# Optimization experiments

Measured on AMD Instinct MI355X. Metric: run time of the kernel, lower is better.

The kernel has to match this reference:

```python
import jax, jax.numpy as jnp
import numpy as np

DIM = 1024
N_HEADS = 16
HEAD_DIM = DIM // N_HEADS
MLP_DIM = 4096
B, L, M = 4, 1024, 1024
EPS = 1e-5


def _mha(q_in, k_in, v_in, mask, wq, wk, wv, wo):
    b, l, d = q_in.shape
    m = k_in.shape[1]
    # torch view(b, l, head_dim, n_heads): split last dim as (head_dim, n_heads)
    q = (q_in @ wq).reshape(b, l, HEAD_DIM, N_HEADS)
    k = (k_in @ wk).reshape(b, m, HEAD_DIM, N_HEADS)
    v = (v_in @ wv).reshape(b, m, HEAD_DIM, N_HEADS)  # computed but unused downstream (source quirk)
    score = jnp.einsum('bldn,bmdn->blmn', q, k)
    # source applies mask BEFORE scaling
    score = jnp.where(mask, jnp.float32(-1e9), score)
    score = score / (HEAD_DIM ** 0.5)
    attn = jax.nn.softmax(score, axis=2)
    # SOURCE QUIRK: second einsum uses k, not v — reproduced faithfully
    x = jnp.einsum('blmn,bmdn->bldn', attn, k)
    x = x.reshape(b, l, d)  # 'b l d n -> b l (d n)'
    return x @ wo


def _layer_norm(x, g, b):
    mu = jnp.mean(x, axis=-1, keepdims=True)
    var = jnp.var(x, axis=-1, keepdims=True)
    return (x - mu) * jax.lax.rsqrt(var + EPS) * g + b


def setup_inputs() -> dict:
    key = jax.random.key(0)
    ks = jax.random.split(key, 16)
    s = 0.02
    inp = {
        'x': jax.random.normal(ks[0], (B, L, DIM), dtype=jnp.float32),
        'enc_output': jax.random.normal(ks[1], (B, M, DIM), dtype=jnp.float32),
        # causal mask: True above diagonal => masked
        'self_attn_mask': jnp.triu(jnp.ones((L, L), dtype=bool), k=1)[None, :, :, None],
        'enc_dec_mask': jnp.zeros((1, L, M, 1), dtype=bool),
        'sa_wq': s * jax.random.normal(ks[2], (DIM, DIM), jnp.float32),
        'sa_wk': s * jax.random.normal(ks[3], (DIM, DIM), jnp.float32),
        'sa_wv': s * jax.random.normal(ks[4], (DIM, DIM), jnp.float32),
        'sa_wo': s * jax.random.normal(ks[5], (DIM, DIM), jnp.float32),
        'ca_wq': s * jax.random.normal(ks[6], (DIM, DIM), jnp.float32),
        'ca_wk': s * jax.random.normal(ks[7], (DIM, DIM), jnp.float32),
        'ca_wv': s * jax.random.normal(ks[8], (DIM, DIM), jnp.float32),
        'ca_wo': s * jax.random.normal(ks[9], (DIM, DIM), jnp.float32),
        'ln1_g': jnp.ones((DIM,), jnp.float32), 'ln1_b': jnp.zeros((DIM,), jnp.float32),
        'ln2_g': jnp.ones((DIM,), jnp.float32), 'ln2_b': jnp.zeros((DIM,), jnp.float32),
        'ln3_g': jnp.ones((DIM,), jnp.float32), 'ln3_b': jnp.zeros((DIM,), jnp.float32),
        'ff_w1': s * jax.random.normal(ks[10], (DIM, MLP_DIM), jnp.float32),
        'ff_b1': jnp.zeros((MLP_DIM,), jnp.float32),
        'ff_w2': s * jax.random.normal(ks[11], (MLP_DIM, DIM), jnp.float32),
        'ff_b2': jnp.zeros((DIM,), jnp.float32),
    }
    return inp


def reference(x, enc_output, self_attn_mask, enc_dec_mask,
              sa_wq, sa_wk, sa_wv, sa_wo,
              ca_wq, ca_wk, ca_wv, ca_wo,
              ln1_g, ln1_b, ln2_g, ln2_b, ln3_g, ln3_b,
              ff_w1, ff_b1, ff_w2, ff_b2):
    # self-attention + residual + LN (dropout = identity in eval)
    h = x + _mha(x, x, x, self_attn_mask, sa_wq, sa_wk, sa_wv, sa_wo)
    h = _layer_norm(h, ln1_g, ln1_b)
    # encoder-decoder attention + residual + LN
    h = h + _mha(h, enc_output, enc_output, enc_dec_mask, ca_wq, ca_wk, ca_wv, ca_wo)
    h = _layer_norm(h, ln2_g, ln2_b)
    # position-wise FFN (gelu, exact erf like torch default) + residual + LN
    ff = jax.nn.gelu(h @ ff_w1 + ff_b1, approximate=False) @ ff_w2 + ff_b2
    h = h + ff
    h = _layer_norm(h, ln3_g, ln3_b)
    return h
```

## Files before the change

### kernel.cpp

```cpp
#include <hip/hip_runtime.h>
#include <hip/hip_bf16.h>
#include <stdint.h>

typedef unsigned short u16;
typedef _Float16 f16x8 __attribute__((ext_vector_type(8)));
typedef float f32x4 __attribute__((ext_vector_type(4)));

#define TOK 4096

__device__ __forceinline__ u16 f2h(float f) {
  _Float16 h = (_Float16)f;
  return __builtin_bit_cast(unsigned short, h);
}
__device__ __forceinline__ float h2f(u16 b) {
  return (float)__builtin_bit_cast(_Float16, b);
}
__device__ __forceinline__ unsigned pack2(float a, float b) {
  return (unsigned)f2h(a) | ((unsigned)f2h(b) << 16);
}
__device__ __forceinline__ void gld16(const u16* g, u16* l) {
  __builtin_amdgcn_global_load_lds(
      (const __attribute__((address_space(1))) void*)g,
      (__attribute__((address_space(3))) void*)l, 16, 0, 0);
}
__device__ __forceinline__ float gelu_fast(float v) {
  float z = 1.5957691216f * v * (1.0f + 0.044715f * v * v);
  return v / (1.0f + __expf(-z));
}

__device__ __forceinline__ void tc_body(const float* W, u16* Wt, int K, int N,
                                        int bx, int by, int tid) {
  __shared__ float tile[32][33];
  int n0 = bx * 32, k0 = by * 32;
  int tx = tid & 31, ty = tid >> 5;
#pragma unroll
  for (int e = 0; e < 4; e++)
    tile[ty + e * 8][tx] = W[(size_t)(k0 + ty + e * 8) * N + n0 + tx];
  __syncthreads();
#pragma unroll
  for (int e = 0; e < 4; e++)
    Wt[(size_t)(n0 + ty + e * 8) * K + k0 + tx] = f2h(tile[tx][ty + e * 8]);
}
__device__ __forceinline__ void cast_body(const float* in, u16* out, int blk, int tid) {
  int i = blk * 256 + tid;
  const float4* p = (const float4*)(in + (size_t)i * 8);
  float4 a = p[0], b = p[1];
  uint4 o;
  o.x = pack2(a.x, a.y); o.y = pack2(a.z, a.w);
  o.z = pack2(b.x, b.y); o.w = pack2(b.z, b.w);
  *(uint4*)(out + (size_t)i * 8) = o;
}

__global__ __launch_bounds__(256) void prep_kernel(
    const float* x, const float* enc, u16* xh, u16* ench,
    const float* W0, const float* W1, const float* W2,
    const float* W3, const float* W4, const float* W5,
    u16* T0, u16* T1, u16* T2, u16* T3, u16* T4, u16* T5,
    const float* Wff1, u16* Tff1, const float* Wff2, u16* Tff2) {
  int blk = blockIdx.x, tid = threadIdx.x;
  if (blk < 2048) { cast_body(x, xh, blk, tid); return; }
  if (blk < 4096) { cast_body(enc, ench, blk - 2048, tid); return; }
  if (blk < 10240) {
    int t = blk - 4096;
    int z = t >> 10, s = t & 1023;
    const float* W; u16* T;
    switch (z) {
      case 0: W = W0; T = T0; break;
      case 1: W = W1; T = T1; break;
      case 2: W = W2; T = T2; break;
      case 3: W = W3; T = T3; break;
      case 4: W = W4; T = T4; break;
      default: W = W5; T = T5; break;
    }
    tc_body(W, T, 1024, 1024, s & 31, s >> 5, tid);
    return;
  }
  if (blk < 14336) {
    int t = blk - 10240;
    tc_body(Wff1, Tff1, 1024, 4096, t & 127, t >> 7, tid);
    return;
  }
  {
    int t = blk - 14336;
    tc_body(Wff2, Tff2, 4096, 1024, t & 31, t >> 5, tid);
  }
}

template <int EPI, int BN, int BK>
__global__ __launch_bounds__((BN == 256) ? 512 : 256)
void gemm_bt_kernel(const u16* __restrict__ A0,
                    const u16* __restrict__ A1,
                    const u16* __restrict__ Bt,
                    u16* __restrict__ Cb0,
                    u16* __restrict__ Cb1,
                    u16* __restrict__ CbT,
                    const float* __restrict__ bias,
                    int M, int N, int K, int KLEN) {
  constexpr int SWM = BK / 8 - 1;
  __shared__ u16 As[2][128 * BK];
  __shared__ u16 Bs[2][BN * BK];
  int tid = threadIdx.x, lane = tid & 63, wid = tid >> 6;
  int gx = gridDim.x, gy = gridDim.y;
  int nwg = gx * gy;
  int flat = blockIdx.x + gx * blockIdx.y;
  int k8 = flat & 7, idx = flat >> 3;
  int bx, by;
  if (gx >= 16) {
    int rx = gx >> 2, ry = gy >> 1;
    int kx = k8 & 3, ky = k8 >> 2;
    bx = kx * rx + idx % rx;
    by = ky * ry + idx / rx;
  } else {
    int widx = k8 * (nwg >> 3) + idx;
    bx = widx % gx;
    by = widx / gx;
  }
  int row0 = by * 128, col0 = bx * BN;
  bool is_k = (EPI == 0) && (col0 >= 1024);
  const u16* A = is_k ? A1 : A0;
  int wm = (BN == 256) ? (wid >> 2) * 64 : (wid >> 1) * 64;
  int wn = (BN == 256) ? (wid & 3) * 64 : (wid & 1) * 64;
  size_t koff = (EPI == 4) ? (size_t)blockIdx.z * KLEN : 0;
  int ra = lane & 15, kg = lane >> 4;

  const u16 *Ab0, *Ab1, *Bb0, *Bb1;
  int srow = 0, ssw = 0;
  if constexpr (BK == 64) {
    srow = wid * 8 + (lane >> 3);
    ssw = (lane & 7) ^ ((srow >> 1) & 7);
    Ab0 = A + (size_t)(row0 + srow) * K + koff + ssw * 8;
    Bb0 = Bt + (size_t)(col0 + srow) * K + koff + ssw * 8;
    Ab1 = nullptr; Bb1 = nullptr;
  } else {
    int sr = tid >> 2;
    int scol = (((tid & 3) ^ ((sr >> 1) & 3)) * 8);
    Ab0 = A + (size_t)(row0 + sr) * K + koff + scol;
    Ab1 = A + (size_t)(row0 + 64 + sr) * K + koff + scol;
    Bb0 = Bt + (size_t)(col0 + sr) * K + koff + scol;
    Bb1 = Bt + (size_t)(col0 + ((BN == 256) ? 128 : 64) + sr) * K + koff + scol;
  }

  f32x4 acc[4][4];
#pragma unroll
  for (int i = 0; i < 4; i++)
#pragma unroll
    for (int j = 0; j < 4; j++) { acc[i][j][0] = 0.f; acc[i][j][1] = 0.f; acc[i][j][2] = 0.f; acc[i][j][3] = 0.f; }
  int KT = KLEN / BK;
  int arow[4], asw[4], brow[4], bsw[4];
#pragma unroll
  for (int i = 0; i < 4; i++) {
    arow[i] = wm + i * 16 + ra;
    asw[i] = (arow[i] >> 1) & SWM;
    brow[i] = wn + i * 16 + ra;
    bsw[i] = (brow[i] >> 1) & SWM;
  }

  auto STAGE = [&](int kt, int buf) {
    if constexpr (BK == 64) {
#pragma unroll
      for (int i = 0; i < 4; i++) {
        gld16(Ab0 + (size_t)i * 32 * K + kt * 64, &As[buf][i * 2048 + wid * 512]);
        gld16(Bb0 + (size_t)i * 32 * K + kt * 64, &Bs[buf][i * 2048 + wid * 512]);
      }
    } else if constexpr (BN == 256) {
      gld16(Ab0 + kt * 32, &As[buf][wid * 512]);
      gld16(Bb0 + kt * 32, &Bs[buf][wid * 512]);
      gld16(Bb1 + kt * 32, &Bs[buf][4096 + wid * 512]);
    } else {
      gld16(Ab0 + kt * 32, &As[buf][wid * 512]);
      gld16(Ab1 + kt * 32, &As[buf][2048 + wid * 512]);
      gld16(Bb0 + kt * 32, &Bs[buf][wid * 512]);
      gld16(Bb1 + kt * 32, &Bs[buf][2048 + wid * 512]);
    }
  };

  STAGE(0, 0);
  __syncthreads();
  int cur = 0;
  for (int kt = 0; kt < KT; ++kt) {
    if (kt + 1 < KT) STAGE(kt + 1, cur ^ 1);
#pragma unroll
    for (int kk = 0; kk < BK / 32; kk++) {
      f16x8 af[4], bfv[4];
#pragma unroll
      for (int i = 0; i < 4; i++)
        af[i] = *(const f16x8*)&As[cur][arow[i] * BK + (((kk * 4 + kg) ^ asw[i]) * 8)];
#pragma unroll
      for (int j = 0; j < 4; j++)
        bfv[j] = *(const f16x8*)&Bs[cur][brow[j] * BK + (((kk * 4 + kg) ^ bsw[j]) * 8)];
#pragma unroll
      for (int i = 0; i < 4; i++)
#pragma unroll
        for (int j = 0; j < 4; j++)
          acc[i][j] = __builtin_amdgcn_mfma_f32_16x16x32_f16(af[i], bfv[j], acc[i][j], 0, 0, 0);
    }
    __syncthreads();
    cur ^= 1;
  }

  int rq = kg * 4;
#pragma unroll
  for (int i = 0; i < 4; i++) {
    int rowb = row0 + wm + i * 16 + rq;
    if (EPI == 0) {
      int b = rowb >> 10, l0 = rowb & 1023;
      int d0 = ((col0 + wn) >> 4) & 63;
      size_t hb = ((size_t)(b * 16 + ra)) * 1024;
      u16* dst = is_k ? Cb1 : Cb0;
      u16 h[4][4];
#pragma unroll
      for (int j = 0; j < 4; j++)
#pragma unroll
        for (int q = 0; q < 4; q++) h[j][q] = f2h(acc[i][j][q]);
#pragma unroll
      for (int q = 0; q < 4; q++) {
        ushort4 hv;
        hv.x = h[0][q]; hv.y = h[1][q]; hv.z = h[2][q]; hv.w = h[3][q];
        *(ushort4*)&dst[(hb + l0 + q) * 64 + d0] = hv;
      }
      if (is_k) {
#pragma unroll
        for (int j = 0; j < 4; j++) {
          uint2 ov;
          ov.x = (unsigned)h[j][0] | ((unsigned)h[j][1] << 16);
          ov.y = (unsigned)h[j][2] | ((unsigned)h[j][3] << 16);
          *(uint2*)&CbT[((size_t)(b * 16 + ra)) * 65536 + ((size_t)(d0 + j)) * 1024 + l0] = ov;
        }
      }
    } else {
#pragma unroll
      for (int j = 0; j < 4; j++) {
        int col = col0 + wn + j * 16 + ra;
        float bval = 0.f;
        if (EPI == 2) bval = bias[col];
        if (EPI == 4 && blockIdx.z == 0 && bias) bval = bias[col];
#pragma unroll
        for (int q = 0; q < 4; q++) {
          int row = rowb + q;
          float v = acc[i][j][q] + bval;
          if (EPI == 2) {
            Cb0[(size_t)row * N + col] = f2h(gelu_fast(v));
          } else {
            Cb0[(size_t)blockIdx.z * M * N + (size_t)row * N + col] = f2h(v);
          }
        }
      }
    }
  }
}

template <bool CAUSAL>
__global__ __launch_bounds__(256) void flash3_kernel(const u16* __restrict__ Qh,
                                                     const u16* __restrict__ Kh,
                                                     const u16* __restrict__ KhT,
                                                     u16* __restrict__ Xtok) {
  const int L = 1024;
  int tid = threadIdx.x, lane = tid & 63, wid = tid >> 6;
  int gx = gridDim.x, nwg = gx * gridDim.y;
  int flat = blockIdx.x + gx * blockIdx.y;
  int widx = (flat & 7) * (nwg >> 3) + (flat >> 3);
  int qt = widx % gx, bh = widx / gx;
  if (CAUSAL) qt = gx - 1 - qt;
  __shared__ u16 Ks[2][4096];
  __shared__ u16 Kt[2][4096];
  __shared__ u16 Ps[4][2048];
  int ra = lane & 15, kg = lane >> 4;
  int rq = kg * 4;
  int wr0 = qt * 128 + wid * 32;
  f16x8 qa[2][2];
#pragma unroll
  for (int i = 0; i < 2; i++) {
    const u16* Qb = Qh + ((size_t)bh * L + wr0 + i * 16 + ra) * 64;
    qa[i][0] = *(const f16x8*)(Qb + kg * 8);
    qa[i][1] = *(const f16x8*)(Qb + 32 + kg * 8);
  }
  f32x4 oacc[2][4];
#pragma unroll
  for (int i = 0; i < 2; i++)
#pragma unroll
    for (int d = 0; d < 4; d++) { oacc[i][d][0] = 0.f; oacc[i][d][1] = 0.f; oacc[i][d][2] = 0.f; oacc[i][d][3] = 0.f; }
  float l_i[2][4];
#pragma unroll
  for (int i = 0; i < 2; i++)
#pragma unroll
    for (int q = 0; q < 4; q++) l_i[i][q] = 0.f;
  int ntiles = CAUSAL ? (2 * qt + 2) : 16;
  int fr = lane >> 3, fc = lane & 7;

#define KSTAGE(mt, buf) do {                                                        \
    {                                                                               \
      int rr = wid * 8 + fr;                                                        \
      int cc = fc ^ fr;                                                             \
      gld16(Kh + ((size_t)bh * L + (mt) * 64 + rr) * 64 + cc * 8, &Ks[buf][wid * 512]);          \
      gld16(KhT + ((size_t)bh * 64 + rr) * L + (size_t)(mt) * 64 + cc * 8, &Kt[buf][wid * 512]); \
    }                                                                               \
    {                                                                               \
      int rr = 32 + wid * 8 + fr;                                                   \
      int cc = fc ^ fr;                                                             \
      gld16(Kh + ((size_t)bh * L + (mt) * 64 + rr) * 64 + cc * 8, &Ks[buf][2048 + wid * 512]);          \
      gld16(KhT + ((size_t)bh * 64 + rr) * L + (size_t)(mt) * 64 + cc * 8, &Kt[buf][2048 + wid * 512]); \
    }                                                                               \
  } while (0)

  KSTAGE(0, 0);
  __syncthreads();
  int cur = 0;
  for (int mt = 0; mt < ntiles; ++mt) {
    if (mt + 1 < ntiles) KSTAGE(mt + 1, cur ^ 1);
    bool active = !(CAUSAL && (wr0 + 31 < mt * 64));
    if (active) {
      bool wmask = CAUSAL && (mt * 64 + 63 > wr0);
      float p[2][4][4];
      __builtin_amdgcn_s_setprio(1);
#pragma unroll
      for (int j = 0; j < 4; j++) {
        int krow = j * 16 + ra;
        int s2 = krow & 7;
        f16x8 kb0 = *(const f16x8*)&Ks[cur][krow * 64 + ((kg ^ s2) * 8)];
        f16x8 kb1 = *(const f16x8*)&Ks[cur][krow * 64 + (((4 + kg) ^ s2) * 8)];
#pragma unroll
        for (int i = 0; i < 2; i++) {
          f32x4 a; a[0] = 0.f; a[1] = 0.f; a[2] = 0.f; a[3] = 0.f;
          a = __builtin_amdgcn_mfma_f32_16x16x32_f16(qa[i][0], kb0, a, 0, 0, 0);
          a = __builtin_amdgcn_mfma_f32_16x16x32_f16(qa[i][1], kb1, a, 0, 0, 0);
#pragma unroll
          for (int q = 0; q < 4; q++) {
            float v = a[q] * 0.125f;
            if (wmask) {
              int rg = wr0 + i * 16 + rq + q;
              int cg = mt * 64 + j * 16 + ra;
              if (cg > rg) v = -1.25e8f;
            }
            p[i][j][q] = __expf(v);
          }
        }
      }
      __builtin_amdgcn_s_setprio(0);
#pragma unroll
      for (int i = 0; i < 2; i++) {
        float rs[4] = {0.f, 0.f, 0.f, 0.f};
#pragma unroll
        for (int j = 0; j < 4; j++)
#pragma unroll
          for (int q = 0; q < 4; q++) rs[q] += p[i][j][q];
#pragma unroll
        for (int off = 1; off < 16; off <<= 1)
#pragma unroll
          for (int q = 0; q < 4; q++) rs[q] += __shfl_xor(rs[q], off);
#pragma unroll
        for (int q = 0; q < 4; q++) l_i[i][q] += rs[q];
      }
#pragma unroll
      for (int i = 0; i < 2; i++)
#pragma unroll
        for (int j = 0; j < 4; j++)
#pragma unroll
          for (int q = 0; q < 4; q++) {
            int prow = i * 16 + rq + q;
            int pcol = j * 16 + ra;
            Ps[wid][prow * 64 + (((pcol >> 3) ^ (prow & 7)) * 8) + (pcol & 7)] = f2h(p[i][j][q]);
          }
      f16x8 pa[2][2];
#pragma unroll
      for (int i = 0; i < 2; i++) {
        int arow = i * 16 + ra;
        int s3 = arow & 7;
        pa[i][0] = *(const f16x8*)&Ps[wid][arow * 64 + ((kg ^ s3) * 8)];
        pa[i][1] = *(const f16x8*)&Ps[wid][arow * 64 + (((4 + kg) ^ s3) * 8)];
      }
      __builtin_amdgcn_s_setprio(1);
#pragma unroll
      for (int d = 0; d < 4; d++) {
        int krow = d * 16 + ra;
        int s4 = krow & 7;
        f16x8 kc0 = *(const f16x8*)&Kt[cur][krow * 64 + ((kg ^ s4) * 8)];
        f16x8 kc1 = *(const f16x8*)&Kt[cur][krow * 64 + (((4 + kg) ^ s4) * 8)];
#pragma unroll
        for (int i = 0; i < 2; i++) {
          oacc[i][d] = __builtin_amdgcn_mfma_f32_16x16x32_f16(pa[i][0], kc0, oacc[i][d], 0, 0, 0);
          oacc[i][d] = __builtin_amdgcn_mfma_f32_16x16x32_f16(pa[i][1], kc1, oacc[i][d], 0, 0, 0);
        }
      }
      __builtin_amdgcn_s_setprio(0);
    }
    __syncthreads();
    cur ^= 1;
  }
#undef KSTAGE
  int b = bh >> 4, nh = bh & 15;
#pragma unroll
  for (int i = 0; i < 2; i++)
#pragma unroll
    for (int q = 0; q < 4; q++) {
      float inv = 1.0f / l_i[i][q];
      int l = wr0 + i * 16 + rq + q;
      size_t rowg = ((size_t)b * 1024 + l) * 1024;
#pragma unroll
      for (int d = 0; d < 4; d++)
        Xtok[rowg + (d * 16 + ra) * 16 + nh] = f2h(oacc[i][d][q] * inv);
    }
}

template <int WRITE_H, int P>
__global__ __launch_bounds__(256) void ln_kernel(const u16* __restrict__ parts,
                                                 const float* __restrict__ res,
                                                 const float* __restrict__ g,
                                                 const float* __restrict__ bb,
                                                 float* __restrict__ outf,
                                                 u16* __restrict__ outh) {
  int row = blockIdx.x, tid = threadIdx.x;
  int lane = tid & 63, wid = tid >> 6;
  size_t base = (size_t)row * 1024 + tid * 4;
  float4 vr = *(const float4*)(res + base);
  float x0 = vr.x, x1 = vr.y, x2 = vr.z, x3 = vr.w;
#pragma unroll
  for (int p = 0; p < P; p++) {
    uint2 v = *(const uint2*)&parts[(size_t)p * 4194304 + base];
    x0 += h2f((u16)v.x);
    x1 += h2f((u16)(v.x >> 16));
    x2 += h2f((u16)v.y);
    x3 += h2f((u16)(v.y >> 16));
  }
  float s = x0 + x1 + x2 + x3;
  float sq = x0 * x0 + x1 * x1 + x2 * x2 + x3 * x3;
#pragma unroll
  for (int off = 1; off < 64; off <<= 1) {
    s += __shfl_xor(s, off);
    sq += __shfl_xor(sq, off);
  }
  __shared__ float red[8];
  if (lane == 0) { red[wid] = s; red[4 + wid] = sq; }
  __syncthreads();
  s = red[0] + red[1] + red[2] + red[3];
  sq = red[4] + red[5] + red[6] + red[7];
  float mean = s * (1.0f / 1024.0f);
  float var = sq * (1.0f / 1024.0f) - mean * mean;
  float rstd = rsqrtf(var + 1e-5f);
  float4 vg = *(const float4*)(g + tid * 4);
  float4 vb = *(const float4*)(bb + tid * 4);
  float y0 = (x0 - mean) * rstd * vg.x + vb.x;
  float y1 = (x1 - mean) * rstd * vg.y + vb.y;
  float y2 = (x2 - mean) * rstd * vg.z + vb.z;
  float y3 = (x3 - mean) * rstd * vg.w + vb.w;
  float4 yo; yo.x = y0; yo.y = y1; yo.z = y2; yo.w = y3;
  *(float4*)(outf + base) = yo;
  if (WRITE_H) {
    uint2 ov; ov.x = pack2(y0, y1); ov.y = pack2(y2, y3);
    *(uint2*)(outh + base) = ov;
  }
}

extern "C" void kernel_launch(void* const* d_in, const int* in_sizes, int n_in,
                              void* d_out, int out_size, void* d_ws, size_t ws_size,
                              hipStream_t stream) {
  (void)in_sizes; (void)n_in; (void)out_size; (void)ws_size;
  const float* x    = (const float*)d_in[0];
  const float* enc  = (const float*)d_in[1];
  const float* sa_wq = (const float*)d_in[4];
  const float* sa_wk = (const float*)d_in[5];
  const float* sa_wo = (const float*)d_in[7];
  const float* ca_wq = (const float*)d_in[8];
  const float* ca_wk = (const float*)d_in[9];
  const float* ca_wo = (const float*)d_in[11];
  const float* ln1g = (const float*)d_in[12];
  const float* ln1b = (const float*)d_in[13];
  const float* ln2g = (const float*)d_in[14];
  const float* ln2b = (const float*)d_in[15];
  const float* ln3g = (const float*)d_in[16];
  const float* ln3b = (const float*)d_in[17];
  const float* ffw1 = (const float*)d_in[18];
  const float* ffb1 = (const float*)d_in[19];
  const float* ffw2 = (const float*)d_in[20];
  const float* ffb2 = (const float*)d_in[21];

  uint8_t* w = (uint8_t*)d_ws;
  const size_t MB = 1024ull * 1024ull;
  u16* wt_saqk = (u16*)(w + 0 * MB);
  u16* wt_sao  = (u16*)(w + 4 * MB);
  u16* wt_caqk = (u16*)(w + 6 * MB);
  u16* wt_cao  = (u16*)(w + 10 * MB);
  u16* wt_ff1  = (u16*)(w + 12 * MB);
  u16* wt_ff2  = (u16*)(w + 20 * MB);
  u16* act_h   = (u16*)(w + 28 * MB);
  u16* enc_h   = (u16*)(w + 36 * MB);
  u16* qhd     = (u16*)(w + 44 * MB);
  u16* khd     = (u16*)(w + 52 * MB);
  u16* khdT    = (u16*)(w + 60 * MB);
  u16* ctxtok  = (u16*)(w + 68 * MB);
  u16* parts   = (u16*)(w + 76 * MB);
  float* hA    = (float*)(w + 108 * MB);
  float* hB    = (float*)(w + 124 * MB);
  u16* ff1h = qhd;

  prep_kernel<<<18432, 256, 0, stream>>>(
      x, enc, act_h, enc_h,
      sa_wq, sa_wk, sa_wo, ca_wq, ca_wk, ca_wo,
      wt_saqk, wt_saqk + 1024 * 1024, wt_sao,
      wt_caqk, wt_caqk + 1024 * 1024, wt_cao,
      ffw1, wt_ff1, ffw2, wt_ff2);

  gemm_bt_kernel<0, 128, 64><<<dim3(16, 32, 1), 256, 0, stream>>>(
      act_h, act_h, wt_saqk, qhd, khd, khdT, nullptr, TOK, 2048, 1024, 1024);
  flash3_kernel<true><<<dim3(8, 64), 256, 0, stream>>>(qhd, khd, khdT, ctxtok);
  gemm_bt_kernel<4, 128, 64><<<dim3(8, 32, 2), 256, 0, stream>>>(
      ctxtok, ctxtok, wt_sao, parts, nullptr, nullptr, nullptr, TOK, 1024, 1024, 512);
  ln_kernel<1, 2><<<4096, 256, 0, stream>>>(parts, x, ln1g, ln1b, hA, act_h);

  gemm_bt_kernel<0, 128, 64><<<dim3(16, 32, 1), 256, 0, stream>>>(
      act_h, enc_h, wt_caqk, qhd, khd, khdT, nullptr, TOK, 2048, 1024, 1024);
  flash3_kernel<false><<<dim3(8, 64), 256, 0, stream>>>(qhd, khd, khdT, ctxtok);
  gemm_bt_kernel<4, 128, 64><<<dim3(8, 32, 2), 256, 0, stream>>>(
      ctxtok, ctxtok, wt_cao, parts, nullptr, nullptr, nullptr, TOK, 1024, 1024, 512);
  ln_kernel<1, 2><<<4096, 256, 0, stream>>>(parts, hA, ln2g, ln2b, hB, act_h);

  gemm_bt_kernel<2, 256, 32><<<dim3(16, 32, 1), 512, 0, stream>>>(
      act_h, act_h, wt_ff1, ff1h, nullptr, nullptr, ffb1, TOK, 4096, 1024, 1024);
  gemm_bt_kernel<4, 128, 64><<<dim3(8, 32, 2), 256, 0, stream>>>(
      ff1h, ff1h, wt_ff2, parts, nullptr, nullptr, ffb2, TOK, 1024, 4096, 2048);
  ln_kernel<0, 2><<<4096, 256, 0, stream>>>(parts, hB, ln3g, ln3b, (float*)d_out, nullptr);
}
```

Measured before the change: 332.4 us.

## Split attention work across 8 waves with 16 query rows each

The flash attention kernel now launches 512 threads (8 waves) per 128-row query tile instead of 4 waves of 32 rows. Each wave handles 16 rows, so the cooperative K/K^T tile staging needs one load pair per thread instead of two. The per-tile row-sum shuffle reduction is deferred to the end, with each lane accumulating partial sums locally. This aims for more latency hiding and less per-tile reduction work, at the cost of each K fragment read from LDS being reused by only one MFMA row block instead of two.

Result: faster. 307.9 us (-7.4%).

```diff
diff --git a/kernel.cpp b/kernel.cpp
--- a/kernel.cpp
+++ b/kernel.cpp
@@ -124,10 +124,9 @@
   int ra = lane & 15, kg = lane >> 4;
 
   const u16 *Ab0, *Ab1, *Bb0, *Bb1;
-  int srow = 0, ssw = 0;
   if constexpr (BK == 64) {
-    srow = wid * 8 + (lane >> 3);
-    ssw = (lane & 7) ^ ((srow >> 1) & 7);
+    int srow = wid * 8 + (lane >> 3);
+    int ssw = (lane & 7) ^ ((srow >> 1) & 7);
     Ab0 = A + (size_t)(row0 + srow) * K + koff + ssw * 8;
     Bb0 = Bt + (size_t)(col0 + srow) * K + koff + ssw * 8;
     Ab1 = nullptr; Bb1 = nullptr;
@@ -250,7 +249,7 @@
 }
 
 template <bool CAUSAL>
-__global__ __launch_bounds__(256) void flash3_kernel(const u16* __restrict__ Qh,
+__global__ __launch_bounds__(512) void flash4_kernel(const u16* __restrict__ Qh,
                                                      const u16* __restrict__ Kh,
                                                      const u16* __restrict__ KhT,
                                                      u16* __restrict__ Xtok) {
@@ -263,43 +262,28 @@
   if (CAUSAL) qt = gx - 1 - qt;
   __shared__ u16 Ks[2][4096];
   __shared__ u16 Kt[2][4096];
-  __shared__ u16 Ps[4][2048];
-  int ra = lane & 15, kg = lane >> 4;
-  int rq = kg * 4;
-  int wr0 = qt * 128 + wid * 32;
-  f16x8 qa[2][2];
-#pragma unroll
-  for (int i = 0; i < 2; i++) {
-    const u16* Qb = Qh + ((size_t)bh * L + wr0 + i * 16 + ra) * 64;
-    qa[i][0] = *(const f16x8*)(Qb + kg * 8);
-    qa[i][1] = *(const f16x8*)(Qb + 32 + kg * 8);
-  }
-  f32x4 oacc[2][4];
-#pragma unroll
-  for (int i = 0; i < 2; i++)
-#pragma unroll
-    for (int d = 0; d < 4; d++) { oacc[i][d][0] = 0.f; oacc[i][d][1] = 0.f; oacc[i][d][2] = 0.f; oacc[i][d][3] = 0.f; }
-  float l_i[2][4];
-#pragma unroll
-  for (int i = 0; i < 2; i++)
-#pragma unroll
-    for (int q = 0; q < 4; q++) l_i[i][q] = 0.f;
+  __shared__ u16 Ps[8][1024];
+  int ra = lane & 15, kg = lane >> 4, rq = kg * 4;
+  int wr0 = qt * 128 + wid * 16;
+  f16x8 qa0, qa1;
+  {
+    const u16* Qb = Qh + ((size_t)bh * L + wr0 + ra) * 64;
+    qa0 = *(const f16x8*)(Qb + kg * 8);
+    qa1 = *(const f16x8*)(Qb + 32 + kg * 8);
+  }
+  f32x4 oacc[4];
+#pragma unroll
+  for (int d = 0; d < 4; d++) { oacc[d][0] = 0.f; oacc[d][1] = 0.f; oacc[d][2] = 0.f; oacc[d][3] = 0.f; }
+  float l_acc[4] = {0.f, 0.f, 0.f, 0.f};
   int ntiles = CAUSAL ? (2 * qt + 2) : 16;
   int fr = lane >> 3, fc = lane & 7;
-
-#define KSTAGE(mt, buf) do {                                                        \
-    {                                                                               \
-      int rr = wid * 8 + fr;                                                        \
-      int cc = fc ^ fr;                                                             \
-      gld16(Kh + ((size_t)bh * L + (mt) * 64 + rr) * 64 + cc * 8, &Ks[buf][wid * 512]);          \
-      gld16(KhT + ((size_t)bh * 64 + rr) * L + (size_t)(mt) * 64 + cc * 8, &Kt[buf][wid * 512]); \
-    }                                                                               \
-    {                                                                               \
-      int rr = 32 + wid * 8 + fr;                                                   \
-      int cc = fc ^ fr;                                                             \
-      gld16(Kh + ((size_t)bh * L + (mt) * 64 + rr) * 64 + cc * 8, &Ks[buf][2048 + wid * 512]);          \
-      gld16(KhT + ((size_t)bh * 64 + rr) * L + (size_t)(mt) * 64 + cc * 8, &Kt[buf][2048 + wid * 512]); \
-    }                                                                               \
+  int rr = wid * 8 + fr;
+  int cc_ = fc ^ (rr & 7);
+  int sw = ra & 7;
+
+#define KSTAGE(mt, buf) do {                                                            \
+    gld16(Kh + ((size_t)bh * L + (mt) * 64 + rr) * 64 + cc_ * 8, &Ks[buf][wid * 512]);  \
+    gld16(KhT + ((size_t)bh * 64 + rr) * L + (size_t)(mt) * 64 + cc_ * 8, &Kt[buf][wid * 512]); \
   } while (0)
 
   KSTAGE(0, 0);
@@ -307,79 +291,52 @@
   int cur = 0;
   for (int mt = 0; mt < ntiles; ++mt) {
     if (mt + 1 < ntiles) KSTAGE(mt + 1, cur ^ 1);
-    bool active = !(CAUSAL && (wr0 + 31 < mt * 64));
+    bool active = !(CAUSAL && (wr0 + 15 < mt * 64));
     if (active) {
       bool wmask = CAUSAL && (mt * 64 + 63 > wr0);
-      float p[2][4][4];
+      float p[4][4];
       __builtin_amdgcn_s_setprio(1);
 #pragma unroll
       for (int j = 0; j < 4; j++) {
         int krow = j * 16 + ra;
-        int s2 = krow & 7;
-        f16x8 kb0 = *(const f16x8*)&Ks[cur][krow * 64 + ((kg ^ s2) * 8)];
-        f16x8 kb1 = *(const f16x8*)&Ks[cur][krow * 64 + (((4 + kg) ^ s2) * 8)];
-#pragma unroll
-        for (int i = 0; i < 2; i++) {
-          f32x4 a; a[0] = 0.f; a[1] = 0.f; a[2] = 0.f; a[3] = 0.f;
-          a = __builtin_amdgcn_mfma_f32_16x16x32_f16(qa[i][0], kb0, a, 0, 0, 0);
-          a = __builtin_amdgcn_mfma_f32_16x16x32_f16(qa[i][1], kb1, a, 0, 0, 0);
-#pragma unroll
-          for (int q = 0; q < 4; q++) {
-            float v = a[q] * 0.125f;
-            if (wmask) {
-              int rg = wr0 + i * 16 + rq + q;
-              int cg = mt * 64 + j * 16 + ra;
-              if (cg > rg) v = -1.25e8f;
-            }
-            p[i][j][q] = __expf(v);
+        f16x8 kb0 = *(const f16x8*)&Ks[cur][krow * 64 + ((kg ^ sw) * 8)];
+        f16x8 kb1 = *(const f16x8*)&Ks[cur][krow * 64 + (((4 + kg) ^ sw) * 8)];
+        f32x4 a; a[0] = 0.f; a[1] = 0.f; a[2] = 0.f; a[3] = 0.f;
+        a = __builtin_amdgcn_mfma_f32_16x16x32_f16(qa0, kb0, a, 0, 0, 0);
+        a = __builtin_amdgcn_mfma_f32_16x16x32_f16(qa1, kb1, a, 0, 0, 0);
+#pragma unroll
+        for (int q = 0; q < 4; q++) {
+          float v = a[q] * 0.125f;
+          if (wmask) {
+            int rg = wr0 + rq + q;
+            int cg = mt * 64 + j * 16 + ra;
+            if (cg > rg) v = -1.25e8f;
           }
+          p[j][q] = __expf(v);
         }
       }
       __builtin_amdgcn_s_setprio(0);
 #pragma unroll
-      for (int i = 0; i < 2; i++) {
-        float rs[4] = {0.f, 0.f, 0.f, 0.f};
-#pragma unroll
-        for (int j = 0; j < 4; j++)
-#pragma unroll
-          for (int q = 0; q < 4; q++) rs[q] += p[i][j][q];
-#pragma unroll
-        for (int off = 1; off < 16; off <<= 1)
-#pragma unroll
-          for (int q = 0; q < 4; q++) rs[q] += __shfl_xor(rs[q], off);
-#pragma unroll
-        for (int q = 0; q < 4; q++) l_i[i][q] += rs[q];
-      }
-#pragma unroll
-      for (int i = 0; i < 2; i++)
-#pragma unroll
-        for (int j = 0; j < 4; j++)
-#pragma unroll
-          for (int q = 0; q < 4; q++) {
-            int prow = i * 16 + rq + q;
-            int pcol = j * 16 + ra;
-            Ps[wid][prow * 64 + (((pcol >> 3) ^ (prow & 7)) * 8) + (pcol & 7)] = f2h(p[i][j][q]);
-          }
-      f16x8 pa[2][2];
-#pragma unroll
-      for (int i = 0; i < 2; i++) {
-        int arow = i * 16 + ra;
-        int s3 = arow & 7;
-        pa[i][0] = *(const f16x8*)&Ps[wid][arow * 64 + ((kg ^ s3) * 8)];
-        pa[i][1] = *(const f16x8*)&Ps[wid][arow * 64 + (((4 + kg) ^ s3) * 8)];
-      }
+      for (int q = 0; q < 4; q++)
+        l_acc[q] += (p[0][q] + p[1][q]) + (p[2][q] + p[3][q]);
+#pragma unroll
+      for (int j = 0; j < 4; j++)
+#pragma unroll
+        for (int q = 0; q < 4; q++) {
+          int prow = rq + q;
+          int pcol = j * 16 + ra;
+          Ps[wid][prow * 64 + (((pcol >> 3) ^ (prow & 7)) * 8) + (pcol & 7)] = f2h(p[j][q]);
+        }
+      f16x8 pa0 = *(const f16x8*)&Ps[wid][ra * 64 + ((kg ^ sw) * 8)];
+      f16x8 pa1 = *(const f16x8*)&Ps[wid][ra * 64 + (((4 + kg) ^ sw) * 8)];
       __builtin_amdgcn_s_setprio(1);
 #pragma unroll
       for (int d = 0; d < 4; d++) {
         int krow = d * 16 + ra;
-        int s4 = krow & 7;
-        f16x8 kc0 = *(const f16x8*)&Kt[cur][krow * 64 + ((kg ^ s4) * 8)];
-        f16x8 kc1 = *(const f16x8*)&Kt[cur][krow * 64 + (((4 + kg) ^ s4) * 8)];
-#pragma unroll
-        for (int i = 0; i < 2; i++) {
-          oacc[i][d] = __builtin_amdgcn_mfma_f32_16x16x32_f16(pa[i][0], kc0, oacc[i][d], 0, 0, 0);
-          oacc[i][d] = __builtin_amdgcn_mfma_f32_16x16x32_f16(pa[i][1], kc1, oacc[i][d], 0, 0, 0);
-        }
+        f16x8 kc0 = *(const f16x8*)&Kt[cur][krow * 64 + ((kg ^ sw) * 8)];
+        f16x8 kc1 = *(const f16x8*)&Kt[cur][krow * 64 + (((4 + kg) ^ sw) * 8)];
+        oacc[d] = __builtin_amdgcn_mfma_f32_16x16x32_f16(pa0, kc0, oacc[d], 0, 0, 0);
+        oacc[d] = __builtin_amdgcn_mfma_f32_16x16x32_f16(pa1, kc1, oacc[d], 0, 0, 0);
       }
       __builtin_amdgcn_s_setprio(0);
     }
@@ -387,18 +344,20 @@
     cur ^= 1;
   }
 #undef KSTAGE
+#pragma unroll
+  for (int off = 1; off < 16; off <<= 1)
+#pragma unroll
+    for (int q = 0; q < 4; q++) l_acc[q] += __shfl_xor(l_acc[q], off);
   int b = bh >> 4, nh = bh & 15;
 #pragma unroll
-  for (int i = 0; i < 2; i++)
-#pragma unroll
-    for (int q = 0; q < 4; q++) {
-      float inv = 1.0f / l_i[i][q];
-      int l = wr0 + i * 16 + rq + q;
-      size_t rowg = ((size_t)b * 1024 + l) * 1024;
-#pragma unroll
-      for (int d = 0; d < 4; d++)
-        Xtok[rowg + (d * 16 + ra) * 16 + nh] = f2h(oacc[i][d][q] * inv);
-    }
+  for (int q = 0; q < 4; q++) {
+    float inv = 1.0f / l_acc[q];
+    int l = wr0 + rq + q;
+    size_t rowg = ((size_t)b * 1024 + l) * 1024;
+#pragma unroll
+    for (int d = 0; d < 4; d++)
+      Xtok[rowg + (d * 16 + ra) * 16 + nh] = f2h(oacc[d][q] * inv);
+  }
 }
 
 template <int WRITE_H, int P>
@@ -501,14 +460,14 @@
 
   gemm_bt_kernel<0, 128, 64><<<dim3(16, 32, 1), 256, 0, stream>>>(
       act_h, act_h, wt_saqk, qhd, khd, khdT, nullptr, TOK, 2048, 1024, 1024);
-  flash3_kernel<true><<<dim3(8, 64), 256, 0, stream>>>(qhd, khd, khdT, ctxtok);
+  flash4_kernel<true><<<dim3(8, 64), 512, 0, stream>>>(qhd, khd, khdT, ctxtok);
   gemm_bt_kernel<4, 128, 64><<<dim3(8, 32, 2), 256, 0, stream>>>(
       ctxtok, ctxtok, wt_sao, parts, nullptr, nullptr, nullptr, TOK, 1024, 1024, 512);
   ln_kernel<1, 2><<<4096, 256, 0, stream>>>(parts, x, ln1g, ln1b, hA, act_h);
 
   gemm_bt_kernel<0, 128, 64><<<dim3(16, 32, 1), 256, 0, stream>>>(
       act_h, enc_h, wt_caqk, qhd, khd, khdT, nullptr, TOK, 2048, 1024, 1024);
-  flash3_kernel<false><<<dim3(8, 64), 256, 0, stream>>>(qhd, khd, khdT, ctxtok);
+  flash4_kernel<false><<<dim3(8, 64), 512, 0, stream>>>(qhd, khd, khdT, ctxtok);
   gemm_bt_kernel<4, 128, 64><<<dim3(8, 32, 2), 256, 0, stream>>>(
       ctxtok, ctxtok, wt_cao, parts, nullptr, nullptr, nullptr, TOK, 1024, 1024, 512);
   ln_kernel<1, 2><<<4096, 256, 0, stream>>>(parts, hA, ln2g, ln2b, hB, act_h);
```
